# Kernel optimization log

Measured on AMD Instinct MI355X. Metric: run time of the kernel, lower is better.

Reference implementation:

```python
import jax, jax.numpy as jnp
import numpy as np

B, Cfi, H, W = 2, 32, 192, 192
Cfp, Cfo, NUM = 1, 2, 16
N = H * W
Ct = Cfo + Cfi + Cfi + Cfp  # 67
EPS = 1e-5


def _bn(x, g, b, m, v):
    # x: (B, C, num, N); per-channel inference batchnorm
    inv = g * jax.lax.rsqrt(v + EPS)
    return x * inv[None, :, None, None] + (b - m * inv)[None, :, None, None]


def _pconv(x, Wt):
    # 1x1 conv as channel contraction: Wt (Cout, Cin), x (B, Cin, num, N)
    return jnp.einsum('oc,bcmn->bomn', Wt, x)


def setup_inputs() -> dict:
    key = jax.random.key(0)
    ks = jax.random.split(key, 32)
    inp = {
        'If': jax.random.normal(ks[0], (B, Cfi, H, W), jnp.float32),
        'Pf': jax.random.normal(ks[1], (B, Cfp, H, W), jnp.float32),
        'Ofnum': jax.random.normal(ks[2], (B, Cfo, NUM, N), jnp.float32),
        'args': jax.random.randint(ks[3], (B, NUM, N), 0, N, jnp.int64),
    }
    def conv_w(k, co, ci):
        return jax.random.normal(k, (co, ci), jnp.float32) * (1.0 / np.sqrt(ci))
    def bn_p(k, c):
        k1, k2 = jax.random.split(k)
        return (jnp.ones((c,), jnp.float32),
                jnp.zeros((c,), jnp.float32),
                jax.random.normal(k1, (c,), jnp.float32) * 0.1,
                jax.random.uniform(k2, (c,), jnp.float32, 0.5, 1.5))
    # convXF: Ct->Cfi, Cfi->Cfi (both BN+GELU)
    inp['W1'] = conv_w(ks[4], Cfi, Ct)
    inp['g1'], inp['b1'], inp['m1'], inp['v1'] = bn_p(ks[5], Cfi)
    inp['W2'] = conv_w(ks[6], Cfi, Cfi)
    inp['g2'], inp['b2'], inp['m2'], inp['v2'] = bn_p(ks[7], Cfi)
    # convXL: Cfi->Cfi (BN+GELU), Cfi->Cfi (BN only)
    inp['W3'] = conv_w(ks[8], Cfi, Cfi)
    inp['g3'], inp['b3'], inp['m3'], inp['v3'] = bn_p(ks[9], Cfi)
    inp['W4'] = conv_w(ks[10], Cfi, Cfi)
    inp['g4'], inp['b4'], inp['m4'], inp['v4'] = bn_p(ks[11], Cfi)
    # coef: Cfi -> 3, with bias
    inp['Wc'] = conv_w(ks[12], 3, Cfi)
    inp['bc'] = jax.random.normal(ks[13], (3,), jnp.float32) * 0.01
    return inp


def reference(If, Pf, Ofnum, args,
              W1, g1, b1, m1, v1,
              W2, g2, b2, m2, v2,
              W3, g3, b3, m3, v3,
              W4, g4, b4, m4, v4,
              Wc, bc):
    gelu = lambda x: jax.nn.gelu(x, approximate=False)
    If_flat = If.reshape(B, Cfi, N)   # (B, Cfi, N)
    Pf_flat = Pf.reshape(B, Cfp, N)   # (B, Cfp, M), M == N here

    # per-batch neighbor gather along flattened spatial dim
    gath = jax.vmap(lambda f, a: f[:, a])  # (C,N),(num,N) -> (C,num,N)
    IPfnum = gath(If_flat, args)            # (B, Cfi, num, N)
    Pfnum = gath(Pf_flat, args)             # (B, Cfp, num, N)
    Ifnum = jnp.broadcast_to(If_flat[:, :, None, :], (B, Cfi, NUM, N))

    X = jnp.concatenate([Ifnum, IPfnum, Pfnum, Ofnum], axis=1)  # (B, Ct, num, N)

    h = gelu(_bn(_pconv(X, W1), g1, b1, m1, v1))
    h = gelu(_bn(_pconv(h, W2), g2, b2, m2, v2))
    l = gelu(_bn(_pconv(h, W3), g3, b3, m3, v3))
    l = _bn(_pconv(l, W4), g4, b4, m4, v4)
    XF = gelu(h + l)

    feat = _pconv(XF, Wc) + bc[None, :, None, None]  # (B, 3, num, N)
    Alpha, Beta, Omega = feat[:, 0:1], feat[:, 1:2], feat[:, 2:3]
    Omega = jax.nn.softmax(Omega, axis=2)
    dout = jnp.sum(((Alpha + 1.0) * Pfnum[:, -1:] + Beta) * Omega,
                   axis=2, keepdims=True)  # (B, 1, 1, N)
    return dout.reshape(B, 1, H, W)
```

## Files before the change

kernel.cpp:

```cpp
#include <hip/hip_runtime.h>
#include <math.h>

#define BB   2
#define CFI  32
#define NN   36864
#define NUMM 16

#define ZOFSU (BB * NN * 16)

typedef __attribute__((ext_vector_type(8))) short short8;
typedef __attribute__((ext_vector_type(4))) float f4;
typedef __attribute__((ext_vector_type(16))) float f16v;
typedef __attribute__((ext_vector_type(4))) unsigned uint4v;
typedef __attribute__((ext_vector_type(2))) unsigned u2v;

static __device__ __forceinline__ f16v mm32(short8 a, short8 b, f16v c) {
    return __builtin_amdgcn_mfma_f32_32x32x16_bf16(a, b, c, 0, 0, 0);
}

template <int CTRL>
static __device__ __forceinline__ float dpp_add(float x) {
    int y = __builtin_amdgcn_update_dpp(0, __builtin_bit_cast(int, x),
                                        CTRL, 0xf, 0xf, true);
    return x + __builtin_bit_cast(float, y);
}
template <int CTRL>
static __device__ __forceinline__ float dpp_max(float x) {
    int y = __builtin_amdgcn_update_dpp(0, __builtin_bit_cast(int, x),
                                        CTRL, 0xf, 0xf, true);
    return fmaxf(x, __builtin_bit_cast(float, y));
}

static __device__ __forceinline__ float gelu_fast(float x) {
    const float x2  = x * x;
    const float q   = fmaf(-0.10294310f, x2, -2.30211813f);
    const float e   = exp2f(q * x);
    const float r   = __builtin_amdgcn_rcpf(e + 1.0f);
    return x * r;
}

static __device__ __forceinline__ unsigned bf16_rne_bits(float x) {
    unsigned u = __builtin_bit_cast(unsigned, x);
    return u + 0x7fffu + ((u >> 16) & 1u);
}
static __device__ __forceinline__ void split_pack(float x0, float x1,
                                                  unsigned& hi, unsigned& lo) {
    unsigned r0 = bf16_rne_bits(x0);
    unsigned r1 = bf16_rne_bits(x1);
    float h0 = __builtin_bit_cast(float, r0 & 0xffff0000u);
    float h1 = __builtin_bit_cast(float, r1 & 0xffff0000u);
    hi = (r0 >> 16) | (r1 & 0xffff0000u);
    unsigned s0 = bf16_rne_bits(x0 - h0);
    unsigned s1 = bf16_rne_bits(x1 - h1);
    lo = (s0 >> 16) | (s1 & 0xffff0000u);
}

static __device__ __forceinline__ unsigned pack2(float a, float b) {
    unsigned ua = __builtin_bit_cast(unsigned, a) + 0x8000u;
    unsigned ub = __builtin_bit_cast(unsigned, b) + 0x8000u;
    return (ua >> 16) | (ub & 0xffff0000u);
}
static __device__ __forceinline__ float bflo(unsigned u) {
    return __builtin_bit_cast(float, u << 16);
}
static __device__ __forceinline__ float bfhi(unsigned u) {
    return __builtin_bit_cast(float, u & 0xffff0000u);
}

union UV { unsigned u[4]; short8 v; };

__global__ __launch_bounds__(256) void yz_kernel(
    const float* __restrict__ If, const float* __restrict__ Pf,
    const float* __restrict__ W1, const float* __restrict__ g1,
    const float* __restrict__ b1, const float* __restrict__ m1,
    const float* __restrict__ v1,
    float* __restrict__ wsYZ)
{
    __shared__ float wy[1024], wz[1024], wp[32], bt1[32];
    for (int i = threadIdx.x; i < 1024; i += 256) {
        int o = i >> 5, c = i & 31;
        float inv = g1[o] * rsqrtf(v1[o] + 1e-5f);
        wy[i] = W1[o * 67 + c]      * inv;
        wz[i] = W1[o * 67 + 32 + c] * inv;
    }
    if (threadIdx.x < 32) {
        int o = threadIdx.x;
        float inv = g1[o] * rsqrtf(v1[o] + 1e-5f);
        wp[o]  = W1[o * 67 + 64] * inv;
        bt1[o] = b1[o] - m1[o] * inv;
    }
    __syncthreads();

    const int r  = threadIdx.x & 3;
    const int p  = blockIdx.x * 64 + (threadIdx.x >> 2);
    const int b  = p / NN, n = p - b * NN;
    const int o0 = r * 8;
    const float* ifp = If + (size_t)b * CFI * NN + n;

    float v[32];
#pragma unroll
    for (int c = 0; c < 32; c++) v[c] = ifp[(size_t)c * NN];
    const float pf = Pf[p];

    float accY[8], accZ[8];
#pragma unroll
    for (int j = 0; j < 8; j++) {
        const float4* wyr = (const float4*)&wy[(o0 + j) * 32];
        const float4* wzr = (const float4*)&wz[(o0 + j) * 32];
        float ay = bt1[o0 + j];
        float az = wp[o0 + j] * pf;
#pragma unroll
        for (int c4 = 0; c4 < 8; c4++) {
            float4 a = wyr[c4], z = wzr[c4];
            ay = fmaf(a.x, v[4 * c4 + 0], ay);  az = fmaf(z.x, v[4 * c4 + 0], az);
            ay = fmaf(a.y, v[4 * c4 + 1], ay);  az = fmaf(z.y, v[4 * c4 + 1], az);
            ay = fmaf(a.z, v[4 * c4 + 2], ay);  az = fmaf(z.z, v[4 * c4 + 2], az);
            ay = fmaf(a.w, v[4 * c4 + 3], ay);  az = fmaf(z.w, v[4 * c4 + 3], az);
        }
        accY[j] = ay; accZ[j] = az;
    }

    unsigned* wsu = (unsigned*)wsYZ;
    u2v yA, yB, zA, zB;
    yA[0] = pack2(accY[0], accY[1]); yA[1] = pack2(accY[2], accY[3]);
    yB[0] = pack2(accY[4], accY[5]); yB[1] = pack2(accY[6], accY[7]);
    zA[0] = pack2(accZ[0], accZ[1]); zA[1] = pack2(accZ[2], accZ[3]);
    zB[0] = pack2(accZ[4], accZ[5]); zB[1] = pack2(accZ[6], accZ[7]);
    *(u2v*)(wsu + (size_t)p * 16 + 2 * r)          = yA;
    *(u2v*)(wsu + (size_t)p * 16 + 8 + 2 * r)      = yB;
    *(u2v*)(wsu + ZOFSU + (size_t)p * 16 + 2 * r)     = zA;
    *(u2v*)(wsu + ZOFSU + (size_t)p * 16 + 8 + 2 * r) = zB;
}

#define LOADL(Lc)                                                             \
    {                                                                         \
        A0l = *(const short8*)&wfrag[(Lc)][0][1][lane + io][0];               \
        A0h = *(const short8*)&wfrag[(Lc)][0][0][lane + io][0];               \
        A1l = *(const short8*)&wfrag[(Lc)][1][1][lane + io][0];               \
        A1h = *(const short8*)&wfrag[(Lc)][1][0][lane + io][0];               \
        bq0 = *(const f4*)&btl[(Lc) * 32 +      4 * hi + 4 * io];             \
        bq1 = *(const f4*)&btl[(Lc) * 32 +  8 + 4 * hi + 4 * io];             \
        bq2 = *(const f4*)&btl[(Lc) * 32 + 16 + 4 * hi + 4 * io];             \
        bq3 = *(const f4*)&btl[(Lc) * 32 + 24 + 4 * hi + 4 * io];             \
    }

#define LAYER_MM(ACCV, BIN0, BIN1)                                            \
    {                                                                         \
        ACCV[0]  = bq0[0]; ACCV[1]  = bq0[1]; ACCV[2]  = bq0[2]; ACCV[3]  = bq0[3]; \
        ACCV[4]  = bq1[0]; ACCV[5]  = bq1[1]; ACCV[6]  = bq1[2]; ACCV[7]  = bq1[3]; \
        ACCV[8]  = bq2[0]; ACCV[9]  = bq2[1]; ACCV[10] = bq2[2]; ACCV[11] = bq2[3]; \
        ACCV[12] = bq3[0]; ACCV[13] = bq3[1]; ACCV[14] = bq3[2]; ACCV[15] = bq3[3]; \
        ACCV = mm32(A0l, BIN0.v, ACCV);                                       \
        ACCV = mm32(A0h, BIN0.v, ACCV);                                       \
        ACCV = mm32(A1l, BIN1.v, ACCV);                                       \
        ACCV = mm32(A1h, BIN1.v, ACCV);                                       \
    }

#define RELAYOUT(SRC, B0V, B1V)                                               \
    {                                                                         \
        B0V.u[0] = pack2(SRC[0],  SRC[1]);                                    \
        B0V.u[1] = pack2(SRC[2],  SRC[3]);                                    \
        B0V.u[2] = pack2(SRC[4],  SRC[5]);                                    \
        B0V.u[3] = pack2(SRC[6],  SRC[7]);                                    \
        B1V.u[0] = pack2(SRC[8],  SRC[9]);                                    \
        B1V.u[1] = pack2(SRC[10], SRC[11]);                                   \
        B1V.u[2] = pack2(SRC[12], SRC[13]);                                   \
        B1V.u[3] = pack2(SRC[14], SRC[15]);                                   \
    }

__global__ __launch_bounds__(256, 4) void main_kernel(
    const float* __restrict__ Pf, const float* __restrict__ Of,
    const int* __restrict__ args,
    const float* __restrict__ W1, const float* __restrict__ g1,
    const float* __restrict__ v1,
    const float* __restrict__ W2, const float* __restrict__ g2,
    const float* __restrict__ b2, const float* __restrict__ m2,
    const float* __restrict__ v2,
    const float* __restrict__ W3, const float* __restrict__ g3,
    const float* __restrict__ b3, const float* __restrict__ m3,
    const float* __restrict__ v3,
    const float* __restrict__ W4, const float* __restrict__ g4,
    const float* __restrict__ b4, const float* __restrict__ m4,
    const float* __restrict__ v4,
    const float* __restrict__ Wc, const float* __restrict__ bc,
    const float* __restrict__ ws, float* __restrict__ out)
{
    __shared__ __align__(16) unsigned wfrag[3][2][2][64][4];
    __shared__ __align__(16) float btl[3 * 32];
    __shared__ __align__(16) float wch[3 * 32];
    __shared__ __align__(16) float w1t[2 * 32];
    __shared__ float bcs[3];
    __shared__ int   izs;

    const float* Ws[3] = {W2, W3, W4};
    const float* gs[3] = {g2, g3, g4};
    const float* vs[3] = {v2, v3, v4};
    const float* bs[3] = {b2, b3, b4};
    const float* ms[3] = {m2, m3, m4};

    for (int idx = threadIdx.x; idx < 1536; idx += 256) {
        int pp  = idx & 3;
        int ln  = (idx >> 2) & 63;
        int kh  = (idx >> 8) & 1;
        int L   = idx >> 9;
        int row = ln & 31;
        int g   = ln >> 5;
        int k   = kh * 16 + 4 * g + 2 * (pp & 1) + 8 * (pp >> 1);
        float inv = gs[L][row] * rsqrtf(vs[L][row] + 1e-5f);
        float w0 = Ws[L][row * 32 + k]     * inv;
        float w1 = Ws[L][row * 32 + k + 1] * inv;
        unsigned hiw, low;
        split_pack(w0, w1, hiw, low);
        wfrag[L][kh][0][ln][pp] = hiw;
        wfrag[L][kh][1][ln][pp] = low;
    }
    if (threadIdx.x < 96) {
        int L = threadIdx.x >> 5, ch = threadIdx.x & 31;
        btl[threadIdx.x] = bs[L][ch] - ms[L][ch] * (gs[L][ch] * rsqrtf(vs[L][ch] + 1e-5f));
        wch[threadIdx.x] = Wc[L * 32 + ch];
    }
    if (threadIdx.x < 64) {
        int t = threadIdx.x >> 5, ch = threadIdx.x & 31;
        float i1 = g1[ch] * rsqrtf(v1[ch] + 1e-5f);
        w1t[threadIdx.x] = W1[ch * 67 + 65 + t] * i1;
    }
    if (threadIdx.x < 3) bcs[threadIdx.x] = bc[threadIdx.x];
    if (threadIdx.x == 0) izs = (int)(args[0] >> 16);
    __syncthreads();

    const unsigned* wsu = (const unsigned*)ws;
    const int lane  = threadIdx.x & 63;
    const int wid   = threadIdx.x >> 6;
    const int m     = lane & 15;
    const int pt    = (lane >> 4) & 1;
    const int hi    = lane >> 5;
    const int q4    = hi << 2;
    const int izero = izs;

    const int base  = blockIdx.x * 32 + wid * 8 + pt;

    uint4v yu0, yu1, zu0, zu1;
    float of0v, of1v, pfg_n;
    int   aI_n;
    {
        const int C0 = base;
        const int b0 = (C0 >= NN) ? 1 : 0;
        const int n0 = C0 - b0 * NN;
        const int a0 = args[(b0 * NUMM + m) * NN + n0];
        of0v = Of[((b0 * 2 + 0) * NUMM + m) * NN + n0];
        of1v = Of[((b0 * 2 + 1) * NUMM + m) * NN + n0];
        pfg_n = Pf[b0 * NN + a0];
        const uint4v* yb = (const uint4v*)(wsu + (size_t)(b0 * NN + n0) * 16 + hi * 8);
        const uint4v* zb = (const uint4v*)(wsu + ZOFSU + (size_t)(b0 * NN + a0) * 16 + hi * 8);
        yu0 = yb[0]; yu1 = yb[1];
        zu0 = zb[0]; zu1 = zb[1];
        const int C1 = (C0 + 2 < BB * NN) ? C0 + 2 : BB * NN - 1;
        const int b1_ = (C1 >= NN) ? 1 : 0;
        const int n1_ = C1 - b1_ * NN;
        aI_n = args[(b1_ * NUMM + m) * NN + n1_];
    }

#pragma unroll 1
    for (int i = 0; i < 4; i++) {
        const int io = i & izero;
        const int C  = base + i * 2;
        const int b  = (C >= NN) ? 1 : 0;
        const int n  = C - b * NN;
        const float pfg = pfg_n;

        short8 A0l, A0h, A1l, A1h;
        f4 bq0, bq1, bq2, bq3;
        LOADL(0);

        f4 wa[4], wb[4];
        wa[0] = *(const f4*)&w1t[q4 + 4 * io];
        wa[1] = *(const f4*)&w1t[8 + q4 + 4 * io];
        wa[2] = *(const f4*)&w1t[16 + q4 + 4 * io];
        wa[3] = *(const f4*)&w1t[24 + q4 + 4 * io];
        wb[0] = *(const f4*)&w1t[32 + q4 + 4 * io];
        wb[1] = *(const f4*)&w1t[40 + q4 + 4 * io];
        wb[2] = *(const f4*)&w1t[48 + q4 + 4 * io];
        wb[3] = *(const f4*)&w1t[56 + q4 + 4 * io];

        float x[16];
#pragma unroll
        for (int q = 0; q < 4; q++) {
            const unsigned ya0 = (q < 2) ? yu0[2 * q]     : yu1[2 * q - 4];
            const unsigned ya1 = (q < 2) ? yu0[2 * q + 1] : yu1[2 * q - 3];
            const unsigned za0 = (q < 2) ? zu0[2 * q]     : zu1[2 * q - 4];
            const unsigned za1 = (q < 2) ? zu0[2 * q + 1] : zu1[2 * q - 3];
            x[4 * q + 0] = fmaf(of1v, wb[q][0], fmaf(of0v, wa[q][0], bflo(ya0) + bflo(za0)));
            x[4 * q + 1] = fmaf(of1v, wb[q][1], fmaf(of0v, wa[q][1], bfhi(ya0) + bfhi(za0)));
            x[4 * q + 2] = fmaf(of1v, wb[q][2], fmaf(of0v, wa[q][2], bflo(ya1) + bflo(za1)));
            x[4 * q + 3] = fmaf(of1v, wb[q][3], fmaf(of0v, wa[q][3], bfhi(ya1) + bfhi(za1)));
        }
#pragma unroll
        for (int j = 0; j < 16; j++) x[j] = gelu_fast(x[j]);
        UV B0, B1;
        RELAYOUT(x, B0, B1);

        {
            const int Cn = (C + 2 < BB * NN) ? C + 2 : BB * NN - 1;
            const int bn = (Cn >= NN) ? 1 : 0;
            const int nn = Cn - bn * NN;
            const uint4v* ybn = (const uint4v*)(wsu + (size_t)(bn * NN + nn) * 16 + hi * 8);
            yu0 = ybn[0]; yu1 = ybn[1];
            of0v = Of[((bn * 2 + 0) * NUMM + m) * NN + nn];
            of1v = Of[((bn * 2 + 1) * NUMM + m) * NN + nn];
            const int aN = aI_n;
            pfg_n = Pf[bn * NN + aN];
            const uint4v* zbn = (const uint4v*)(wsu + ZOFSU + (size_t)(bn * NN + aN) * 16 + hi * 8);
            zu0 = zbn[0]; zu1 = zbn[1];
            const int Ca = (C + 4 < BB * NN) ? C + 4 : BB * NN - 1;
            const int ba = (Ca >= NN) ? 1 : 0;
            const int na = Ca - ba * NN;
            aI_n = args[(ba * NUMM + m) * NN + na];
        }

        f16v acc;
        LAYER_MM(acc, B0, B1);
        LOADL(1);
        float h2g[16];
#pragma unroll
        for (int r = 0; r < 16; r++) h2g[r] = gelu_fast(acc[r]);
        RELAYOUT(h2g, B0, B1);

        LAYER_MM(acc, B0, B1);
        LOADL(2);
        float h3g[16];
#pragma unroll
        for (int r = 0; r < 16; r++) h3g[r] = gelu_fast(acc[r]);
        RELAYOUT(h3g, B0, B1);

        LAYER_MM(acc, B0, B1);

        float pa = 0.0f, pb = 0.0f, po = 0.0f;
#pragma unroll
        for (int q = 0; q < 4; q++) {
            const f4 wAq = *(const f4*)&wch[      8 * q + q4 + 4 * io];
            const f4 wBq = *(const f4*)&wch[32 +  8 * q + q4 + 4 * io];
            const f4 wOq = *(const f4*)&wch[64 +  8 * q + q4 + 4 * io];
#pragma unroll
            for (int r2 = 0; r2 < 4; r2++) {
                float xf = gelu_fast(h2g[4 * q + r2] + acc[4 * q + r2]);
                pa = fmaf(wAq[r2], xf, pa);
                pb = fmaf(wBq[r2], xf, pb);
                po = fmaf(wOq[r2], xf, po);
            }
        }
        pa += __shfl_xor(pa, 32, 64);
        pb += __shfl_xor(pb, 32, 64);
        po += __shfl_xor(po, 32, 64);

        const float alpha = pa + bcs[0];
        const float beta_ = pb + bcs[1];
        const float omega = po + bcs[2];
        const float val = fmaf(alpha + 1.0f, pfg, beta_);

        float mx = dpp_max<0xB1>(omega);
        mx = dpp_max<0x4E>(mx);
        mx = dpp_max<0x141>(mx);
        mx = dpp_max<0x140>(mx);
        const float e = __expf(omega - mx);
        float S = e, T = val * e;
        S = dpp_add<0xB1>(S);   T = dpp_add<0xB1>(T);
        S = dpp_add<0x4E>(S);   T = dpp_add<0x4E>(T);
        S = dpp_add<0x141>(S);  T = dpp_add<0x141>(T);
        S = dpp_add<0x140>(S);  T = dpp_add<0x140>(T);

        if ((lane & 15) == 0 && lane < 32)
            out[b * NN + n] = T * __builtin_amdgcn_rcpf(S);
    }
}

extern "C" void kernel_launch(void* const* d_in, const int* in_sizes, int n_in,
                              void* d_out, int out_size, void* d_ws, size_t ws_size,
                              hipStream_t stream) {
    const float* If    = (const float*)d_in[0];
    const float* Pf    = (const float*)d_in[1];
    const float* Of    = (const float*)d_in[2];
    const int*   args  = (const int*)d_in[3];
    const float* W1    = (const float*)d_in[4];
    const float* g1    = (const float*)d_in[5];
    const float* b1    = (const float*)d_in[6];
    const float* m1    = (const float*)d_in[7];
    const float* v1    = (const float*)d_in[8];
    const float* W2    = (const float*)d_in[9];
    const float* g2    = (const float*)d_in[10];
    const float* b2    = (const float*)d_in[11];
    const float* m2    = (const float*)d_in[12];
    const float* v2    = (const float*)d_in[13];
    const float* W3    = (const float*)d_in[14];
    const float* g3    = (const float*)d_in[15];
    const float* b3    = (const float*)d_in[16];
    const float* m3    = (const float*)d_in[17];
    const float* v3    = (const float*)d_in[18];
    const float* W4    = (const float*)d_in[19];
    const float* g4    = (const float*)d_in[20];
    const float* b4    = (const float*)d_in[21];
    const float* m4    = (const float*)d_in[22];
    const float* v4    = (const float*)d_in[23];
    const float* Wc    = (const float*)d_in[24];
    const float* bc    = (const float*)d_in[25];

    float* ws  = (float*)d_ws;
    float* out = (float*)d_out;

    yz_kernel<<<(BB * NN) / 64, 256, 0, stream>>>(
        If, Pf, W1, g1, b1, m1, v1, ws);

    main_kernel<<<(BB * NN) / 32, 256, 0, stream>>>(
        Pf, Of, args,
        W1, g1, v1,
        W2, g2, b2, m2, v2,
        W3, g3, b3, m3, v3,
        W4, g4, b4, m4, v4,
        Wc, bc, ws, out);
}
```

Measured before the change: 226.7 us.

## Fuse GELU with bf16 packing and keep h2 packed to cut register pressure

Computes GELU and packs to bf16 pairs in the same loop, so the full float arrays (x, h2g, h3g) are no longer kept live. The residual h2 is read back from the packed bf16 copy instead of the fp32 values, and the layer-1 weights are loaded per iteration instead of all up front. Launch bounds go from 4 to 5 waves per SIMD to take advantage of the lower register count. Using the bf16-rounded h2 in the residual add slightly changes numerics, and the tighter launch bound could force spills.

```diff
diff --git a/kernel.cpp b/kernel.cpp
--- a/kernel.cpp
+++ b/kernel.cpp
@@ -156,19 +156,20 @@
         ACCV = mm32(A1h, BIN1.v, ACCV);                                       \
     }
 
-#define RELAYOUT(SRC, B0V, B1V)                                               \
+#define GELU_PACK(ACCV, B0V, B1V)                                             \
     {                                                                         \
-        B0V.u[0] = pack2(SRC[0],  SRC[1]);                                    \
-        B0V.u[1] = pack2(SRC[2],  SRC[3]);                                    \
-        B0V.u[2] = pack2(SRC[4],  SRC[5]);                                    \
-        B0V.u[3] = pack2(SRC[6],  SRC[7]);                                    \
-        B1V.u[0] = pack2(SRC[8],  SRC[9]);                                    \
-        B1V.u[1] = pack2(SRC[10], SRC[11]);                                   \
-        B1V.u[2] = pack2(SRC[12], SRC[13]);                                   \
-        B1V.u[3] = pack2(SRC[14], SRC[15]);                                   \
-    }
-
-__global__ __launch_bounds__(256, 4) void main_kernel(
+        _Pragma("unroll")                                                     \
+        for (int k = 0; k < 4; k++) {                                         \
+            float t0 = gelu_fast(ACCV[2 * k]);                                \
+            float t1 = gelu_fast(ACCV[2 * k + 1]);                            \
+            B0V.u[k] = pack2(t0, t1);                                         \
+            float t2 = gelu_fast(ACCV[8 + 2 * k]);                            \
+            float t3 = gelu_fast(ACCV[8 + 2 * k + 1]);                        \
+            B1V.u[k] = pack2(t2, t3);                                         \
+        }                                                                     \
+    }
+
+__global__ __launch_bounds__(256, 5) void main_kernel(
     const float* __restrict__ Pf, const float* __restrict__ Of,
     const int* __restrict__ args,
     const float* __restrict__ W1, const float* __restrict__ g1,
@@ -272,32 +273,25 @@
         f4 bq0, bq1, bq2, bq3;
         LOADL(0);
 
-        f4 wa[4], wb[4];
-        wa[0] = *(const f4*)&w1t[q4 + 4 * io];
-        wa[1] = *(const f4*)&w1t[8 + q4 + 4 * io];
-        wa[2] = *(const f4*)&w1t[16 + q4 + 4 * io];
-        wa[3] = *(const f4*)&w1t[24 + q4 + 4 * io];
-        wb[0] = *(const f4*)&w1t[32 + q4 + 4 * io];
-        wb[1] = *(const f4*)&w1t[40 + q4 + 4 * io];
-        wb[2] = *(const f4*)&w1t[48 + q4 + 4 * io];
-        wb[3] = *(const f4*)&w1t[56 + q4 + 4 * io];
-
-        float x[16];
+        UV B0, B1;
 #pragma unroll
         for (int q = 0; q < 4; q++) {
+            const f4 waq = *(const f4*)&w1t[8 * q + q4 + 4 * io];
+            const f4 wbq = *(const f4*)&w1t[32 + 8 * q + q4 + 4 * io];
             const unsigned ya0 = (q < 2) ? yu0[2 * q]     : yu1[2 * q - 4];
             const unsigned ya1 = (q < 2) ? yu0[2 * q + 1] : yu1[2 * q - 3];
             const unsigned za0 = (q < 2) ? zu0[2 * q]     : zu1[2 * q - 4];
             const unsigned za1 = (q < 2) ? zu0[2 * q + 1] : zu1[2 * q - 3];
-            x[4 * q + 0] = fmaf(of1v, wb[q][0], fmaf(of0v, wa[q][0], bflo(ya0) + bflo(za0)));
-            x[4 * q + 1] = fmaf(of1v, wb[q][1], fmaf(of0v, wa[q][1], bfhi(ya0) + bfhi(za0)));
-            x[4 * q + 2] = fmaf(of1v, wb[q][2], fmaf(of0v, wa[q][2], bflo(ya1) + bflo(za1)));
-            x[4 * q + 3] = fmaf(of1v, wb[q][3], fmaf(of0v, wa[q][3], bfhi(ya1) + bfhi(za1)));
+            float t0 = fmaf(of1v, wbq[0], fmaf(of0v, waq[0], bflo(ya0) + bflo(za0)));
+            float t1 = fmaf(of1v, wbq[1], fmaf(of0v, waq[1], bfhi(ya0) + bfhi(za0)));
+            float t2 = fmaf(of1v, wbq[2], fmaf(of0v, waq[2], bflo(ya1) + bflo(za1)));
+            float t3 = fmaf(of1v, wbq[3], fmaf(of0v, waq[3], bfhi(ya1) + bfhi(za1)));
+            t0 = gelu_fast(t0); t1 = gelu_fast(t1);
+            t2 = gelu_fast(t2); t3 = gelu_fast(t3);
+            const unsigned lo2 = pack2(t0, t1), hi2 = pack2(t2, t3);
+            if (q < 2) { B0.u[2 * q] = lo2; B0.u[2 * q + 1] = hi2; }
+            else       { B1.u[2 * q - 4] = lo2; B1.u[2 * q - 3] = hi2; }
         }
-#pragma unroll
-        for (int j = 0; j < 16; j++) x[j] = gelu_fast(x[j]);
-        UV B0, B1;
-        RELAYOUT(x, B0, B1);
 
         {
             const int Cn = (C + 2 < BB * NN) ? C + 2 : BB * NN - 1;
@@ -320,17 +314,13 @@
         f16v acc;
         LAYER_MM(acc, B0, B1);
         LOADL(1);
-        float h2g[16];
-#pragma unroll
-        for (int r = 0; r < 16; r++) h2g[r] = gelu_fast(acc[r]);
-        RELAYOUT(h2g, B0, B1);
+        UV P0, P1;
+        GELU_PACK(acc, P0, P1);
+        B0 = P0; B1 = P1;
 
         LAYER_MM(acc, B0, B1);
         LOADL(2);
-        float h3g[16];
-#pragma unroll
-        for (int r = 0; r < 16; r++) h3g[r] = gelu_fast(acc[r]);
-        RELAYOUT(h3g, B0, B1);
+        GELU_PACK(acc, B0, B1);
 
         LAYER_MM(acc, B0, B1);
 
@@ -340,13 +330,20 @@
             const f4 wAq = *(const f4*)&wch[      8 * q + q4 + 4 * io];
             const f4 wBq = *(const f4*)&wch[32 +  8 * q + q4 + 4 * io];
             const f4 wOq = *(const f4*)&wch[64 +  8 * q + q4 + 4 * io];
-#pragma unroll
-            for (int r2 = 0; r2 < 4; r2++) {
-                float xf = gelu_fast(h2g[4 * q + r2] + acc[4 * q + r2]);
-                pa = fmaf(wAq[r2], xf, pa);
-                pb = fmaf(wBq[r2], xf, pb);
-                po = fmaf(wOq[r2], xf, po);
-            }
+            const unsigned pu0 = (q < 2) ? P0.u[2 * q]     : P1.u[2 * q - 4];
+            const unsigned pu1 = (q < 2) ? P0.u[2 * q + 1] : P1.u[2 * q - 3];
+            const float h20 = bflo(pu0), h21 = bfhi(pu0);
+            const float h22 = bflo(pu1), h23 = bfhi(pu1);
+            float xf0 = gelu_fast(h20 + acc[4 * q + 0]);
+            float xf1 = gelu_fast(h21 + acc[4 * q + 1]);
+            float xf2 = gelu_fast(h22 + acc[4 * q + 2]);
+            float xf3 = gelu_fast(h23 + acc[4 * q + 3]);
+            pa = fmaf(wAq[0], xf0, pa); pa = fmaf(wAq[1], xf1, pa);
+            pa = fmaf(wAq[2], xf2, pa); pa = fmaf(wAq[3], xf3, pa);
+            pb = fmaf(wBq[0], xf0, pb); pb = fmaf(wBq[1], xf1, pb);
+            pb = fmaf(wBq[2], xf2, pb); pb = fmaf(wBq[3], xf3, pb);
+            po = fmaf(wOq[0], xf0, po); po = fmaf(wOq[1], xf1, po);
+            po = fmaf(wOq[2], xf2, po); po = fmaf(wOq[3], xf3, po);
         }
         pa += __shfl_xor(pa, 32, 64);
         pb += __shfl_xor(pb, 32, 64);
```

After: 225.7 us (median of 2 runs). About the same (-0.4%).
